# Optimization experiments

Hardware: AMD Instinct MI355X
Metric: run time of the kernel (lower is better)

Reference implementation:

```python
import jax, jax.numpy as jnp
import numpy as np

DIM = 128
HEADS = 4
K = 7          # neighborhood kernel size
MLP_RATIO = 4
EPS = 1e-5


def setup_inputs() -> dict:
    key = jax.random.key(0)
    ks = jax.random.split(key, 8)
    B, H, W, C = 4, 64, 64, DIM
    hid = C * MLP_RATIO
    s = lambda k, shape: jax.random.normal(k, shape, jnp.float32) * 0.02
    return {
        "x": jax.random.normal(ks[0], (B, H, W, C), jnp.float32),
        "ln1_g": jnp.ones((C,), jnp.float32),
        "ln1_b": jnp.zeros((C,), jnp.float32),
        "qkv_w": s(ks[1], (C, 3 * C)),
        "qkv_b": jnp.zeros((3 * C,), jnp.float32),
        "rpb": s(ks[2], (HEADS, 2 * K - 1, 2 * K - 1)),
        "proj_w": s(ks[3], (C, C)),
        "proj_b": jnp.zeros((C,), jnp.float32),
        "ln2_g": jnp.ones((C,), jnp.float32),
        "ln2_b": jnp.zeros((C,), jnp.float32),
        "fc1_w": s(ks[4], (C, hid)),
        "fc1_b": jnp.zeros((hid,), jnp.float32),
        "fc2_w": s(ks[5], (hid, C)),
        "fc2_b": jnp.zeros((C,), jnp.float32),
    }


def _ln(x, g, b):
    m = jnp.mean(x, axis=-1, keepdims=True)
    v = jnp.mean(jnp.square(x - m), axis=-1, keepdims=True)
    return (x - m) * jax.lax.rsqrt(v + EPS) * g + b


def _neigh_idx(L, k):
    # NATTEN border-clamped neighborhood: start = clamp(i - k//2, 0, L-k)
    i = jnp.arange(L)
    start = jnp.clip(i - k // 2, 0, L - k)
    idx = start[:, None] + jnp.arange(k)[None, :]        # [L, k] key positions
    rel = idx - i[:, None] + (k - 1)                     # [L, k] rpb indices in [0, 2k-2]
    return idx, rel


def _neighborhood_attention(x, qkv_w, qkv_b, rpb, proj_w, proj_b):
    B, H, W, C = x.shape
    nh, hd = HEADS, C // HEADS
    scale = hd ** -0.5
    qkv = (x @ qkv_w + qkv_b).reshape(B, H, W, 3, nh, hd)
    qkv = qkv.transpose(3, 0, 4, 1, 2, 5)                # [3, B, nh, H, W, hd]
    q, k_, v = qkv[0] * scale, qkv[1], qkv[2]
    ih, rh = _neigh_idx(H, K)
    iw, rw = _neigh_idx(W, K)
    # gather 7x7 neighborhoods: [B, nh, H, K, W, K, hd]
    kg = k_[:, :, ih][:, :, :, :, iw]
    vg = v[:, :, ih][:, :, :, :, iw]
    attn = jnp.einsum('bnywc,bnykxjc->bnyxkj', q, kg)    # [B, nh, H, W, K, K]
    bias = rpb[:, rh][:, :, :, rw]                       # [nh, H, K, W, K]
    attn = attn + bias.transpose(0, 1, 3, 2, 4)[None]
    a = jax.nn.softmax(attn.reshape(B, nh, H, W, K * K), axis=-1)
    a = a.reshape(B, nh, H, W, K, K)
    out = jnp.einsum('bnyxkj,bnykxjc->bnyxc', a, vg)     # [B, nh, H, W, hd]
    out = out.transpose(0, 2, 3, 1, 4).reshape(B, H, W, C)
    return out @ proj_w + proj_b


def reference(x, ln1_g, ln1_b, qkv_w, qkv_b, rpb, proj_w, proj_b,
              ln2_g, ln2_b, fc1_w, fc1_b, fc2_w, fc2_b):
    h = x + _neighborhood_attention(_ln(x, ln1_g, ln1_b), qkv_w, qkv_b, rpb, proj_w, proj_b)
    y = _ln(h, ln2_g, ln2_b)
    y = jax.nn.gelu(y @ fc1_w + fc1_b, approximate=False) @ fc2_w + fc2_b
    return h + y
```

## Files before the change

kernel.cpp:

```cpp
#include <hip/hip_runtime.h>
#include <math.h>

#define TOKS 16384
#define CDIM 128
#define NH 4
#define HD 32
#define HID 512
#define QSCALE 0.17677669529663687f
#define LEPS 1e-5f

typedef const float* fp;
typedef const unsigned short* bfp16;
typedef __attribute__((ext_vector_type(8))) short bf16x8;
typedef __attribute__((ext_vector_type(4))) float f32x4;

__device__ inline unsigned int bfp2(float a, float b) {
    unsigned int ua = __float_as_uint(a); ua = (ua + 0x7FFFu + ((ua >> 16) & 1u)) >> 16;
    unsigned int ub = __float_as_uint(b); ub = (ub + 0x7FFFu + ((ub >> 16) & 1u)) >> 16;
    return ua | (ub << 16);
}
__device__ inline unsigned short bf1(float a) {
    unsigned int u = __float_as_uint(a);
    return (unsigned short)((u + 0x7FFFu + ((u >> 16) & 1u)) >> 16);
}
__device__ inline float lo16(unsigned int u) { return __uint_as_float(u << 16); }
__device__ inline float hi16(unsigned int u) { return __uint_as_float(u & 0xFFFF0000u); }

__global__ __launch_bounds__(256) void prep(fp qw, fp pw, fp f1w, fp f2w,
                                            fp x, fp g, fp b,
                                            unsigned short* __restrict__ wt,
                                            unsigned short* __restrict__ xn) {
    const int bid = blockIdx.x;
    if (bid < 768) {
        int e = bid * 256 + threadIdx.x;
        float v;
        if (e < 49152)       { int n = e >> 7,  k = e & 127;          v = qw[(size_t)k * 384 + n]; }
        else if (e < 65536)  { int i = e - 49152;  int n = i >> 7, k = i & 127; v = pw[(size_t)k * 128 + n]; }
        else if (e < 131072) { int i = e - 65536;  int n = i >> 7, k = i & 127; v = f1w[(size_t)k * 512 + n]; }
        else                 { int i = e - 131072; int n = i >> 9, k = i & 511; v = f2w[(size_t)k * 128 + n]; }
        wt[e] = bf1(v);
    } else {
        const int t = threadIdx.x;
        const int row = (bid - 768) * 8 + (t >> 5);
        const int l = t & 31;
        const float4 v = *(const float4*)(x + (size_t)row * CDIM + l * 4);
        float s = v.x + v.y + v.z + v.w;
        float q = v.x * v.x + v.y * v.y + v.z * v.z + v.w * v.w;
#pragma unroll
        for (int m = 16; m >= 1; m >>= 1) { s += __shfl_xor(s, m); q += __shfl_xor(q, m); }
        float mu = s * (1.f / 128.f);
        float rs = rsqrtf(q * (1.f / 128.f) - mu * mu + LEPS);
        const float4 gv = *(const float4*)(g + l * 4);
        const float4 bv = *(const float4*)(b + l * 4);
        float a0 = (v.x - mu) * rs * gv.x + bv.x, a1 = (v.y - mu) * rs * gv.y + bv.y;
        float a2 = (v.z - mu) * rs * gv.z + bv.z, a3 = (v.w - mu) * rs * gv.w + bv.w;
        uint2 o; o.x = bfp2(a0, a1); o.y = bfp2(a2, a3);
        *(uint2*)(xn + (size_t)row * CDIM + l * 4) = o;
    }
}


__global__ __launch_bounds__(256) void k1_mfma(bfp16 xn, bfp16 wt0, fp wb,
                                               float* __restrict__ qb,
                                               unsigned short* __restrict__ kvb) {
    __shared__ unsigned int lds[12288];
    const int m0 = blockIdx.x * 128;
    const int nb = blockIdx.y * 64;
    const int tid = threadIdx.x;
#pragma unroll
    for (int i = 0; i < 8; i++) {
        int slot = tid + i * 256;
        int m = slot >> 4, c16 = slot & 15;
        const uint4 v4 = *(const uint4*)(xn + (size_t)(m0 + m) * CDIM + c16 * 8);
        *(uint4*)&lds[m * 64 + (c16 ^ (m & 15)) * 4] = v4;
    }
#pragma unroll
    for (int i = 0; i < 4; i++) {
        int slot = tid + i * 256;
        int n = slot >> 4, c16 = slot & 15;
        const uint4 v4 = *(const uint4*)(wt0 + (size_t)(nb + n) * 128 + c16 * 8);
        *(uint4*)&lds[8192 + n * 64 + (c16 ^ (n & 15)) * 4] = v4;
    }
    __syncthreads();

    const int lane = tid & 63, wid = tid >> 6, quad = lane >> 4, l16 = lane & 15;
    f32x4 acc[2][4];
#pragma unroll
    for (int mt = 0; mt < 2; mt++)
#pragma unroll
        for (int nt = 0; nt < 4; nt++) acc[mt][nt] = (f32x4){0.f, 0.f, 0.f, 0.f};
#pragma unroll
    for (int kk = 0; kk < 4; kk++) {
        int c = kk * 4 + quad;
        bf16x8 a0 = *(bf16x8*)&lds[(wid * 32 + l16) * 64 + (c ^ l16) * 4];
        bf16x8 a1 = *(bf16x8*)&lds[(wid * 32 + 16 + l16) * 64 + (c ^ l16) * 4];
#pragma unroll
        for (int nt = 0; nt < 4; nt++) {
            bf16x8 bf = *(bf16x8*)&lds[8192 + (nt * 16 + l16) * 64 + (c ^ l16) * 4];
            acc[0][nt] = __builtin_amdgcn_mfma_f32_16x16x32_bf16(a0, bf, acc[0][nt], 0, 0, 0);
            acc[1][nt] = __builtin_amdgcn_mfma_f32_16x16x32_bf16(a1, bf, acc[1][nt], 0, 0, 0);
        }
    }
#pragma unroll
    for (int nt = 0; nt < 4; nt++) {
        int col = nb + nt * 16 + l16;
        float bias = wb[col];
#pragma unroll
        for (int mt = 0; mt < 2; mt++)
#pragma unroll
            for (int r = 0; r < 4; r++) {
                int row = m0 + wid * 32 + mt * 16 + quad * 4 + r;
                float vres = acc[mt][nt][r] + bias;
                if (col < 128)
                    qb[(size_t)row * 128 + col] = vres * QSCALE;
                else if (col < 256)
                    kvb[(size_t)row * 256 + (col - 128)] = bf1(vres);
                else
                    kvb[(size_t)row * 256 + 128 + (col - 256)] = bf1(vres);
            }
    }
}

__global__ __launch_bounds__(256) void k2_attn(const float* __restrict__ qb,
                                               const unsigned short* __restrict__ kvb,
                                               fp rpb, unsigned short* __restrict__ attnb) {
    const int gid = blockIdx.x * 256 + threadIdx.x;
    const int d = gid & 3;
    const int g = (gid >> 2) & 3;
    const int head = (gid >> 4) & 3;
    const int token = gid >> 6;
    const int bb = token >> 12;
    const int y = (token >> 6) & 63;
    const int xx = token & 63;
    const int sy = min(max(y - 3, 0), 57);
    const int sx = min(max(xx - 3, 0), 57);

    const int koff = head * HD + d * 8;
    float q[8];
    {
        const float4* qp = (const float4*)(qb + (size_t)token * 128 + koff);
        float4 q0 = qp[0], q1 = qp[1];
        q[0] = q0.x; q[1] = q0.y; q[2] = q0.z; q[3] = q0.w;
        q[4] = q1.x; q[5] = q1.y; q[6] = q1.z; q[7] = q1.w;
    }

    const float* rp = rpb + head * 169 + (sy - y + 6) * 13 + (sx - xx + 6);
    const int nbase = (bb << 12) + sy * 64 + sx;

    float sc[13];
#pragma unroll
    for (int i = 0; i < 13; i++) {
        int n = g * 13 + i;
        bool ok = n < 49;
        int nn = ok ? n : 48;
        int dy = nn / 7, dx = nn - dy * 7;
        const uint4 kk = *(const uint4*)(kvb + (size_t)(nbase + dy * 64 + dx) * 256 + koff);
        float s = q[0] * lo16(kk.x) + q[1] * hi16(kk.x)
                + q[2] * lo16(kk.y) + q[3] * hi16(kk.y)
                + q[4] * lo16(kk.z) + q[5] * hi16(kk.z)
                + q[6] * lo16(kk.w) + q[7] * hi16(kk.w);
        s += __shfl_xor(s, 1);
        s += __shfl_xor(s, 2);
        sc[i] = ok ? (s + rp[dy * 13 + dx]) : -1e30f;
    }
    float mx = sc[0];
#pragma unroll
    for (int l = 1; l < 13; l++) mx = fmaxf(mx, sc[l]);
    mx = fmaxf(mx, __shfl_xor(mx, 4));
    mx = fmaxf(mx, __shfl_xor(mx, 8));
    float sum = 0.f;
#pragma unroll
    for (int l = 0; l < 13; l++) { sc[l] = __expf(sc[l] - mx); sum += sc[l]; }
    sum += __shfl_xor(sum, 4);
    sum += __shfl_xor(sum, 8);
    float inv = 1.f / sum;

    float o[8];
#pragma unroll
    for (int i = 0; i < 8; i++) o[i] = 0.f;
#pragma unroll
    for (int i = 0; i < 13; i++) {
        int n = g * 13 + i;
        int nn = (n < 49) ? n : 48;
        int dy = nn / 7, dx = nn - dy * 7;
        float p = sc[i] * inv;
        const uint4 vv = *(const uint4*)(kvb + (size_t)(nbase + dy * 64 + dx) * 256 + 128 + koff);
        o[0] += p * lo16(vv.x); o[1] += p * hi16(vv.x);
        o[2] += p * lo16(vv.y); o[3] += p * hi16(vv.y);
        o[4] += p * lo16(vv.z); o[5] += p * hi16(vv.z);
        o[6] += p * lo16(vv.w); o[7] += p * hi16(vv.w);
    }
#pragma unroll
    for (int i = 0; i < 8; i++) {
        o[i] += __shfl_xor(o[i], 4);
        o[i] += __shfl_xor(o[i], 8);
    }
    if (g == 0) {
        uint4 ov;
        ov.x = bfp2(o[0], o[1]); ov.y = bfp2(o[2], o[3]);
        ov.z = bfp2(o[4], o[5]); ov.w = bfp2(o[6], o[7]);
        *(uint4*)(attnb + (size_t)token * 128 + koff) = ov;
    }
}

__global__ __launch_bounds__(256) void k3_mfma(bfp16 attnb, fp x, bfp16 wt1, fp pb,
                                               fp g2, fp b2,
                                               float* __restrict__ h,
                                               unsigned short* __restrict__ hn) {
    __shared__ unsigned int lds[12288];
    const int m0 = blockIdx.x * 64;
    const int tid = threadIdx.x;
#pragma unroll
    for (int i = 0; i < 4; i++) {
        int slot = tid + i * 256;
        int m = slot >> 4, c16 = slot & 15;
        const uint4 v4 = *(const uint4*)(attnb + (size_t)(m0 + m) * CDIM + c16 * 8);
        *(uint4*)&lds[m * 64 + (c16 ^ (m & 15)) * 4] = v4;
    }
#pragma unroll
    for (int i = 0; i < 8; i++) {
        int slot = tid + i * 256;
        int n = slot >> 4, c16 = slot & 15;
        const uint4 v4 = *(const uint4*)(wt1 + (size_t)n * 128 + c16 * 8);
        *(uint4*)&lds[4096 + n * 64 + (c16 ^ (n & 15)) * 4] = v4;
    }
    __syncthreads();

    const int lane = tid & 63, wid = tid >> 6, quad = lane >> 4, l16 = lane & 15;
    const int mrow = wid * 16 + l16;
    f32x4 acc[8];
#pragma unroll
    for (int nt = 0; nt < 8; nt++) acc[nt] = (f32x4){0.f, 0.f, 0.f, 0.f};
#pragma unroll
    for (int kk = 0; kk < 4; kk++) {
        int c = kk * 4 + quad;
        bf16x8 a = *(bf16x8*)&lds[mrow * 64 + (c ^ l16) * 4];
#pragma unroll
        for (int nt = 0; nt < 8; nt++) {
            bf16x8 bf = *(bf16x8*)&lds[4096 + (nt * 16 + l16) * 64 + (c ^ l16) * 4];
            acc[nt] = __builtin_amdgcn_mfma_f32_16x16x32_bf16(a, bf, acc[nt], 0, 0, 0);
        }
    }
    float s[4] = {0.f, 0.f, 0.f, 0.f}, q[4] = {0.f, 0.f, 0.f, 0.f};
#pragma unroll
    for (int nt = 0; nt < 8; nt++) {
        int col = nt * 16 + l16;
        float bias = pb[col];
#pragma unroll
        for (int r = 0; r < 4; r++) {
            int row = m0 + wid * 16 + quad * 4 + r;
            float hv = x[(size_t)row * CDIM + col] + acc[nt][r] + bias;
            h[(size_t)row * CDIM + col] = hv;
            acc[nt][r] = hv;
            s[r] += hv; q[r] += hv * hv;
        }
    }
#pragma unroll
    for (int m = 1; m <= 8; m <<= 1) {
#pragma unroll
        for (int r = 0; r < 4; r++) {
            s[r] += __shfl_xor(s[r], m);
            q[r] += __shfl_xor(q[r], m);
        }
    }
    float mu[4], rs[4];
#pragma unroll
    for (int r = 0; r < 4; r++) {
        mu[r] = s[r] * (1.f / 128.f);
        rs[r] = rsqrtf(q[r] * (1.f / 128.f) - mu[r] * mu[r] + LEPS);
    }
#pragma unroll
    for (int nt = 0; nt < 8; nt++) {
        int col = nt * 16 + l16;
        float gg = g2[col], bb = b2[col];
#pragma unroll
        for (int r = 0; r < 4; r++) {
            int row = m0 + wid * 16 + quad * 4 + r;
            hn[(size_t)row * CDIM + col] = bf1((acc[nt][r] - mu[r]) * rs[r] * gg + bb);
        }
    }
}

__global__ __launch_bounds__(256) void k4_mfma(bfp16 hn, bfp16 wt2, fp wb,
                                               unsigned short* __restrict__ y1) {
    __shared__ unsigned int lds[12288];
    const int m0 = blockIdx.x * 128;
    const int nb = blockIdx.y * 64;
    const int tid = threadIdx.x;
#pragma unroll
    for (int i = 0; i < 8; i++) {
        int slot = tid + i * 256;
        int m = slot >> 4, c16 = slot & 15;
        const uint4 v4 = *(const uint4*)(hn + (size_t)(m0 + m) * CDIM + c16 * 8);
        *(uint4*)&lds[m * 64 + (c16 ^ (m & 15)) * 4] = v4;
    }
#pragma unroll
    for (int i = 0; i < 4; i++) {
        int slot = tid + i * 256;
        int n = slot >> 4, c16 = slot & 15;
        const uint4 v4 = *(const uint4*)(wt2 + (size_t)(nb + n) * 128 + c16 * 8);
        *(uint4*)&lds[8192 + n * 64 + (c16 ^ (n & 15)) * 4] = v4;
    }
    __syncthreads();

    const int lane = tid & 63, wid = tid >> 6, quad = lane >> 4, l16 = lane & 15;
    f32x4 acc[2][4];
#pragma unroll
    for (int mt = 0; mt < 2; mt++)
#pragma unroll
        for (int nt = 0; nt < 4; nt++) acc[mt][nt] = (f32x4){0.f, 0.f, 0.f, 0.f};
#pragma unroll
    for (int kk = 0; kk < 4; kk++) {
        int c = kk * 4 + quad;
        bf16x8 a0 = *(bf16x8*)&lds[(wid * 32 + l16) * 64 + (c ^ l16) * 4];
        bf16x8 a1 = *(bf16x8*)&lds[(wid * 32 + 16 + l16) * 64 + (c ^ l16) * 4];
#pragma unroll
        for (int nt = 0; nt < 4; nt++) {
            bf16x8 bf = *(bf16x8*)&lds[8192 + (nt * 16 + l16) * 64 + (c ^ l16) * 4];
            acc[0][nt] = __builtin_amdgcn_mfma_f32_16x16x32_bf16(a0, bf, acc[0][nt], 0, 0, 0);
            acc[1][nt] = __builtin_amdgcn_mfma_f32_16x16x32_bf16(a1, bf, acc[1][nt], 0, 0, 0);
        }
    }
#pragma unroll
    for (int nt = 0; nt < 4; nt++) {
        int col = nb + nt * 16 + l16;
        float bias = wb[col];
#pragma unroll
        for (int mt = 0; mt < 2; mt++)
#pragma unroll
            for (int r = 0; r < 4; r++) {
                int row = m0 + wid * 32 + mt * 16 + quad * 4 + r;
                float z = acc[mt][nt][r] + bias;
                y1[(size_t)row * HID + col] = bf1(0.5f * z * (1.f + erff(z * 0.70710678118654752f)));
            }
    }
}

__global__ __launch_bounds__(256) void k5_mfma(bfp16 y1, fp h, bfp16 wt3, fp wb,
                                               float* __restrict__ out) {
    __shared__ unsigned int lds[12288];
    const int m0 = blockIdx.x * 128;
    const int nb = blockIdx.y * 64;
    const int tid = threadIdx.x;
    const int lane = tid & 63, wid = tid >> 6, quad = lane >> 4, l16 = lane & 15;
    f32x4 acc[2][4];
#pragma unroll
    for (int mt = 0; mt < 2; mt++)
#pragma unroll
        for (int nt = 0; nt < 4; nt++) acc[mt][nt] = (f32x4){0.f, 0.f, 0.f, 0.f};

    for (int kc = 0; kc < 4; kc++) {
        if (kc) __syncthreads();
#pragma unroll
        for (int i = 0; i < 8; i++) {
            int slot = tid + i * 256;
            int m = slot >> 4, c16 = slot & 15;
            const uint4 v4 = *(const uint4*)(y1 + (size_t)(m0 + m) * HID + kc * 128 + c16 * 8);
            *(uint4*)&lds[m * 64 + (c16 ^ (m & 15)) * 4] = v4;
        }
#pragma unroll
        for (int i = 0; i < 4; i++) {
            int slot = tid + i * 256;
            int n = slot >> 4, c16 = slot & 15;
            const uint4 v4 = *(const uint4*)(wt3 + (size_t)(nb + n) * 512 + kc * 128 + c16 * 8);
            *(uint4*)&lds[8192 + n * 64 + (c16 ^ (n & 15)) * 4] = v4;
        }
        __syncthreads();
#pragma unroll
        for (int kk = 0; kk < 4; kk++) {
            int c = kk * 4 + quad;
            bf16x8 a0 = *(bf16x8*)&lds[(wid * 32 + l16) * 64 + (c ^ l16) * 4];
            bf16x8 a1 = *(bf16x8*)&lds[(wid * 32 + 16 + l16) * 64 + (c ^ l16) * 4];
#pragma unroll
            for (int nt = 0; nt < 4; nt++) {
                bf16x8 bf = *(bf16x8*)&lds[8192 + (nt * 16 + l16) * 64 + (c ^ l16) * 4];
                acc[0][nt] = __builtin_amdgcn_mfma_f32_16x16x32_bf16(a0, bf, acc[0][nt], 0, 0, 0);
                acc[1][nt] = __builtin_amdgcn_mfma_f32_16x16x32_bf16(a1, bf, acc[1][nt], 0, 0, 0);
            }
        }
    }
#pragma unroll
    for (int nt = 0; nt < 4; nt++) {
        int col = nb + nt * 16 + l16;
        float bias = wb[col];
#pragma unroll
        for (int mt = 0; mt < 2; mt++)
#pragma unroll
            for (int r = 0; r < 4; r++) {
                int row = m0 + wid * 32 + mt * 16 + quad * 4 + r;
                out[(size_t)row * CDIM + col] = h[(size_t)row * CDIM + col] + acc[mt][nt][r] + bias;
            }
    }
}

extern "C" void kernel_launch(void* const* d_in, const int* in_sizes, int n_in,
                              void* d_out, int out_size, void* d_ws, size_t ws_size,
                              hipStream_t stream) {
    fp x      = (fp)d_in[0];
    fp ln1_g  = (fp)d_in[1];
    fp ln1_b  = (fp)d_in[2];
    fp qkv_w  = (fp)d_in[3];
    fp qkv_b  = (fp)d_in[4];
    fp rpb    = (fp)d_in[5];
    fp proj_w = (fp)d_in[6];
    fp proj_b = (fp)d_in[7];
    fp ln2_g  = (fp)d_in[8];
    fp ln2_b  = (fp)d_in[9];
    fp fc1_w  = (fp)d_in[10];
    fp fc1_b  = (fp)d_in[11];
    fp fc2_w  = (fp)d_in[12];
    fp fc2_b  = (fp)d_in[13];
    float* out = (float*)d_out;

    float* ws = (float*)d_ws;
    float* h  = ws;
    unsigned short* xn = (unsigned short*)(h + (size_t)TOKS * CDIM);
    unsigned short* hn = xn + (size_t)TOKS * CDIM;
    float* qb = (float*)(hn + (size_t)TOKS * CDIM);
    unsigned short* kvb   = (unsigned short*)(qb + (size_t)TOKS * CDIM);
    unsigned short* attnb = kvb + (size_t)TOKS * 256;
    unsigned short* wt    = attnb + (size_t)TOKS * CDIM;
    unsigned short* y1    = (unsigned short*)qb;

    unsigned short* wt0 = wt;
    unsigned short* wt1 = wt + 49152;
    unsigned short* wt2 = wt + 65536;
    unsigned short* wt3 = wt + 131072;

    prep<<<768 + TOKS / 8, 256, 0, stream>>>(qkv_w, proj_w, fc1_w, fc2_w, x, ln1_g, ln1_b, wt, xn);
    k1_mfma<<<dim3(TOKS / 128, 6), 256, 0, stream>>>(xn, wt0, qkv_b, qb, kvb);
    k2_attn<<<TOKS * NH * 16 / 256, 256, 0, stream>>>(qb, kvb, rpb, attnb);
    k3_mfma<<<TOKS / 64, 256, 0, stream>>>(attnb, x, wt1, proj_b, ln2_g, ln2_b, h, hn);
    k4_mfma<<<dim3(TOKS / 128, 8), 256, 0, stream>>>(hn, wt2, fc1_b, y1);
    k5_mfma<<<dim3(TOKS / 128, 2), 256, 0, stream>>>(y1, h, wt3, fc2_b, out);
}
```

Before: 148.9 us.

## Fuse fc1+GELU and fc2 into one MLP kernel keeping hidden activations in LDS

Replaces the separate fc1+GELU and fc2 kernels with a single 512-thread kernel per 64-token tile. The GELU output for all 512 hidden channels stays in shared memory (swizzled), so the bf16 y1 intermediate is never written to or read from global memory. fc1 weight chunks are register-prefetched and double-buffered in LDS, and fc2 weight chunks are register-prefetched across the K loop. The cost is a large LDS footprint (112 KB per block) that limits occupancy, and every block now re-reads the full fc1 and fc2 weights.

Result: slower. 170.3 us (+14.4%).

```diff
diff --git a/kernel.cpp b/kernel.cpp
--- a/kernel.cpp
+++ b/kernel.cpp
@@ -59,7 +59,6 @@
     }
 }
 
-
 __global__ __launch_bounds__(256) void k1_mfma(bfp16 xn, bfp16 wt0, fp wb,
                                                float* __restrict__ qb,
                                                unsigned short* __restrict__ kvb) {
@@ -281,115 +280,124 @@
     }
 }
 
-__global__ __launch_bounds__(256) void k4_mfma(bfp16 hn, bfp16 wt2, fp wb,
-                                               unsigned short* __restrict__ y1) {
-    __shared__ unsigned int lds[12288];
-    const int m0 = blockIdx.x * 128;
-    const int nb = blockIdx.y * 64;
+__global__ __launch_bounds__(512) void kmlp(bfp16 hn, bfp16 wt2, fp b1, bfp16 wt3, fp b2,
+                                            fp h, float* __restrict__ out) {
+    __shared__ unsigned int lds[28672];
+    const int m0 = blockIdx.x * 64;
     const int tid = threadIdx.x;
 #pragma unroll
-    for (int i = 0; i < 8; i++) {
-        int slot = tid + i * 256;
+    for (int i = 0; i < 2; i++) {
+        int slot = tid + i * 512;
         int m = slot >> 4, c16 = slot & 15;
         const uint4 v4 = *(const uint4*)(hn + (size_t)(m0 + m) * CDIM + c16 * 8);
-        *(uint4*)&lds[m * 64 + (c16 ^ (m & 15)) * 4] = v4;
-    }
-#pragma unroll
-    for (int i = 0; i < 4; i++) {
-        int slot = tid + i * 256;
+        *(uint4*)&lds[m * 64 + ((c16 ^ (m & 15)) << 2)] = v4;
+    }
+#pragma unroll
+    for (int i = 0; i < 2; i++) {
+        int slot = tid + i * 512;
         int n = slot >> 4, c16 = slot & 15;
-        const uint4 v4 = *(const uint4*)(wt2 + (size_t)(nb + n) * 128 + c16 * 8);
-        *(uint4*)&lds[8192 + n * 64 + (c16 ^ (n & 15)) * 4] = v4;
+        const uint4 v4 = *(const uint4*)(wt2 + (size_t)n * 128 + c16 * 8);
+        *(uint4*)&lds[4096 + n * 64 + ((c16 ^ (n & 15)) << 2)] = v4;
     }
     __syncthreads();
 
     const int lane = tid & 63, wid = tid >> 6, quad = lane >> 4, l16 = lane & 15;
-    f32x4 acc[2][4];
-#pragma unroll
-    for (int mt = 0; mt < 2; mt++)
-#pragma unroll
-        for (int nt = 0; nt < 4; nt++) acc[mt][nt] = (f32x4){0.f, 0.f, 0.f, 0.f};
-#pragma unroll
-    for (int kk = 0; kk < 4; kk++) {
-        int c = kk * 4 + quad;
-        bf16x8 a0 = *(bf16x8*)&lds[(wid * 32 + l16) * 64 + (c ^ l16) * 4];
-        bf16x8 a1 = *(bf16x8*)&lds[(wid * 32 + 16 + l16) * 64 + (c ^ l16) * 4];
-#pragma unroll
-        for (int nt = 0; nt < 4; nt++) {
-            bf16x8 bf = *(bf16x8*)&lds[8192 + (nt * 16 + l16) * 64 + (c ^ l16) * 4];
-            acc[0][nt] = __builtin_amdgcn_mfma_f32_16x16x32_bf16(a0, bf, acc[0][nt], 0, 0, 0);
-            acc[1][nt] = __builtin_amdgcn_mfma_f32_16x16x32_bf16(a1, bf, acc[1][nt], 0, 0, 0);
-        }
-    }
-#pragma unroll
-    for (int nt = 0; nt < 4; nt++) {
-        int col = nb + nt * 16 + l16;
-        float bias = wb[col];
-#pragma unroll
-        for (int mt = 0; mt < 2; mt++)
-#pragma unroll
-            for (int r = 0; r < 4; r++) {
-                int row = m0 + wid * 32 + mt * 16 + quad * 4 + r;
-                float z = acc[mt][nt][r] + bias;
-                y1[(size_t)row * HID + col] = bf1(0.5f * z * (1.f + erff(z * 0.70710678118654752f)));
-            }
-    }
-}
-
-__global__ __launch_bounds__(256) void k5_mfma(bfp16 y1, fp h, bfp16 wt3, fp wb,
-                                               float* __restrict__ out) {
-    __shared__ unsigned int lds[12288];
-    const int m0 = blockIdx.x * 128;
-    const int nb = blockIdx.y * 64;
-    const int tid = threadIdx.x;
-    const int lane = tid & 63, wid = tid >> 6, quad = lane >> 4, l16 = lane & 15;
-    f32x4 acc[2][4];
-#pragma unroll
-    for (int mt = 0; mt < 2; mt++)
-#pragma unroll
-        for (int nt = 0; nt < 4; nt++) acc[mt][nt] = (f32x4){0.f, 0.f, 0.f, 0.f};
-
-    for (int kc = 0; kc < 4; kc++) {
-        if (kc) __syncthreads();
-#pragma unroll
-        for (int i = 0; i < 8; i++) {
-            int slot = tid + i * 256;
-            int m = slot >> 4, c16 = slot & 15;
-            const uint4 v4 = *(const uint4*)(y1 + (size_t)(m0 + m) * HID + kc * 128 + c16 * 8);
-            *(uint4*)&lds[m * 64 + (c16 ^ (m & 15)) * 4] = v4;
-        }
-#pragma unroll
-        for (int i = 0; i < 4; i++) {
-            int slot = tid + i * 256;
-            int n = slot >> 4, c16 = slot & 15;
-            const uint4 v4 = *(const uint4*)(wt3 + (size_t)(nb + n) * 512 + kc * 128 + c16 * 8);
-            *(uint4*)&lds[8192 + n * 64 + (c16 ^ (n & 15)) * 4] = v4;
-        }
-        __syncthreads();
+    const int ht = wid & 3;
+    const int tt0 = (wid >> 2) << 1;
+
+    for (int ch = 0; ch < 8; ch++) {
+        const int cur = 4096 + ((ch & 1) << 11);
+        uint4 pf0, pf1;
+        if (ch < 7) {
+            int s0 = tid, s1 = tid + 512;
+            pf0 = *(const uint4*)(wt2 + (size_t)((ch + 1) * 64 + (s0 >> 4)) * 128 + (s0 & 15) * 8);
+            pf1 = *(const uint4*)(wt2 + (size_t)((ch + 1) * 64 + (s1 >> 4)) * 128 + (s1 & 15) * 8);
+        }
+        f32x4 acc0 = (f32x4){0.f, 0.f, 0.f, 0.f}, acc1 = (f32x4){0.f, 0.f, 0.f, 0.f};
 #pragma unroll
         for (int kk = 0; kk < 4; kk++) {
             int c = kk * 4 + quad;
-            bf16x8 a0 = *(bf16x8*)&lds[(wid * 32 + l16) * 64 + (c ^ l16) * 4];
-            bf16x8 a1 = *(bf16x8*)&lds[(wid * 32 + 16 + l16) * 64 + (c ^ l16) * 4];
-#pragma unroll
-            for (int nt = 0; nt < 4; nt++) {
-                bf16x8 bf = *(bf16x8*)&lds[8192 + (nt * 16 + l16) * 64 + (c ^ l16) * 4];
-                acc[0][nt] = __builtin_amdgcn_mfma_f32_16x16x32_bf16(a0, bf, acc[0][nt], 0, 0, 0);
-                acc[1][nt] = __builtin_amdgcn_mfma_f32_16x16x32_bf16(a1, bf, acc[1][nt], 0, 0, 0);
+            bf16x8 wf = *(bf16x8*)&lds[cur + (ht * 16 + l16) * 64 + ((c ^ l16) << 2)];
+            bf16x8 x0 = *(bf16x8*)&lds[(tt0 * 16 + l16) * 64 + ((c ^ l16) << 2)];
+            bf16x8 x1 = *(bf16x8*)&lds[((tt0 + 1) * 16 + l16) * 64 + ((c ^ l16) << 2)];
+            acc0 = __builtin_amdgcn_mfma_f32_16x16x32_bf16(wf, x0, acc0, 0, 0, 0);
+            acc1 = __builtin_amdgcn_mfma_f32_16x16x32_bf16(wf, x1, acc1, 0, 0, 0);
+        }
+        const int hidb = ch * 64 + ht * 16 + quad * 4;
+        const float4 bb = *(const float4*)(b1 + hidb);
+        const int c16y = hidb >> 3;
+        const int woff = (quad & 1) << 1;
+#pragma unroll
+        for (int t = 0; t < 2; t++) {
+            f32x4 a = t ? acc1 : acc0;
+            int row = (tt0 + t) * 16 + l16;
+            float z0 = a[0] + bb.x, z1 = a[1] + bb.y, z2 = a[2] + bb.z, z3 = a[3] + bb.w;
+            float g0 = 0.5f * z0 * (1.f + erff(z0 * 0.70710678118654752f));
+            float g1 = 0.5f * z1 * (1.f + erff(z1 * 0.70710678118654752f));
+            float g2v = 0.5f * z2 * (1.f + erff(z2 * 0.70710678118654752f));
+            float g3 = 0.5f * z3 * (1.f + erff(z3 * 0.70710678118654752f));
+            uint2 val; val.x = bfp2(g0, g1); val.y = bfp2(g2v, g3);
+            *(uint2*)&lds[12288 + row * 256 + ((c16y ^ (row & 15)) << 2) + woff] = val;
+        }
+        if (ch < 7) {
+            int base = 4096 + (((ch + 1) & 1) << 11);
+            int s0 = tid, s1 = tid + 512;
+            *(uint4*)&lds[base + (s0 >> 4) * 64 + ((((s0 & 15) ^ ((s0 >> 4) & 15))) << 2)] = pf0;
+            *(uint4*)&lds[base + (s1 >> 4) * 64 + ((((s1 & 15) ^ ((s1 >> 4) & 15))) << 2)] = pf1;
+        }
+        __syncthreads();
+    }
+
+    const int mt = wid >> 1;
+    const int nb0 = (wid & 1) << 2;
+    f32x4 acc[4];
+#pragma unroll
+    for (int j = 0; j < 4; j++) acc[j] = (f32x4){0.f, 0.f, 0.f, 0.f};
+
+    uint4 wreg[4];
+#pragma unroll
+    for (int i = 0; i < 4; i++) {
+        int slot = tid + i * 512;
+        wreg[i] = *(const uint4*)(wt3 + (size_t)(slot >> 4) * 512 + (slot & 15) * 8);
+    }
+    for (int kc = 0; kc < 4; kc++) {
+#pragma unroll
+        for (int i = 0; i < 4; i++) {
+            int slot = tid + i * 512;
+            int n = slot >> 4, c16 = slot & 15;
+            *(uint4*)&lds[4096 + n * 64 + ((c16 ^ (n & 15)) << 2)] = wreg[i];
+        }
+        __syncthreads();
+        if (kc < 3) {
+#pragma unroll
+            for (int i = 0; i < 4; i++) {
+                int slot = tid + i * 512;
+                wreg[i] = *(const uint4*)(wt3 + (size_t)(slot >> 4) * 512 + (kc + 1) * 128 + (slot & 15) * 8);
             }
         }
-    }
-#pragma unroll
-    for (int nt = 0; nt < 4; nt++) {
-        int col = nb + nt * 16 + l16;
-        float bias = wb[col];
-#pragma unroll
-        for (int mt = 0; mt < 2; mt++)
-#pragma unroll
-            for (int r = 0; r < 4; r++) {
-                int row = m0 + wid * 32 + mt * 16 + quad * 4 + r;
-                out[(size_t)row * CDIM + col] = h[(size_t)row * CDIM + col] + acc[mt][nt][r] + bias;
+#pragma unroll
+        for (int kk = 0; kk < 4; kk++) {
+            int c = kk * 4 + quad;
+            int row = mt * 16 + l16;
+            int cc = kc * 16 + c;
+            bf16x8 a = *(bf16x8*)&lds[12288 + row * 256 + ((cc ^ l16) << 2)];
+#pragma unroll
+            for (int j = 0; j < 4; j++) {
+                bf16x8 bfr = *(bf16x8*)&lds[4096 + ((nb0 + j) * 16 + l16) * 64 + ((c ^ l16) << 2)];
+                acc[j] = __builtin_amdgcn_mfma_f32_16x16x32_bf16(a, bfr, acc[j], 0, 0, 0);
             }
+        }
+        __syncthreads();
+    }
+#pragma unroll
+    for (int j = 0; j < 4; j++) {
+        int col = (nb0 + j) * 16 + l16;
+        float bias = b2[col];
+#pragma unroll
+        for (int r = 0; r < 4; r++) {
+            int row = m0 + mt * 16 + quad * 4 + r;
+            out[(size_t)row * CDIM + col] = h[(size_t)row * CDIM + col] + acc[j][r] + bias;
+        }
     }
 }
 
@@ -420,7 +428,6 @@
     unsigned short* kvb   = (unsigned short*)(qb + (size_t)TOKS * CDIM);
     unsigned short* attnb = kvb + (size_t)TOKS * 256;
     unsigned short* wt    = attnb + (size_t)TOKS * CDIM;
-    unsigned short* y1    = (unsigned short*)qb;
 
     unsigned short* wt0 = wt;
     unsigned short* wt1 = wt + 49152;
@@ -431,6 +438,5 @@
     k1_mfma<<<dim3(TOKS / 128, 6), 256, 0, stream>>>(xn, wt0, qkv_b, qb, kvb);
     k2_attn<<<TOKS * NH * 16 / 256, 256, 0, stream>>>(qb, kvb, rpb, attnb);
     k3_mfma<<<TOKS / 64, 256, 0, stream>>>(attnb, x, wt1, proj_b, ln2_g, ln2_b, h, hn);
-    k4_mfma<<<dim3(TOKS / 128, 8), 256, 0, stream>>>(hn, wt2, fc1_b, y1);
-    k5_mfma<<<dim3(TOKS / 128, 2), 256, 0, stream>>>(y1, h, wt3, fc2_b, out);
-}
+    kmlp<<<TOKS / 64, 512, 0, stream>>>(hn, wt2, fc1_b, wt3, fc2_b, h, out);
+}
```

## Fuse LN1 into QKV GEMM and restructure MLP GEMMs to full-width row tiles

Applied to the files above, without the earlier changes.

LayerNorm1 moves out of the prep kernel and into k1, which normalizes its 64-row tile of x directly into LDS. k1 and k4 now use 512-thread blocks that keep the A tile resident and loop over all N chunks, double-buffering weight chunks through registers and LDS. k5 uses 64-row tiles covering all 128 output columns. The aim is to drop the xn round trip through global memory and the repeated A-tile reloads across grid columns, at the cost of fewer, longer blocks and more serialized per-block work.

Result: slower. 153.5 us (+3.1%).

```diff
diff --git a/kernel.cpp b/kernel.cpp
--- a/kernel.cpp
+++ b/kernel.cpp
@@ -27,90 +27,91 @@
 __device__ inline float hi16(unsigned int u) { return __uint_as_float(u & 0xFFFF0000u); }
 
 __global__ __launch_bounds__(256) void prep(fp qw, fp pw, fp f1w, fp f2w,
-                                            fp x, fp g, fp b,
-                                            unsigned short* __restrict__ wt,
-                                            unsigned short* __restrict__ xn) {
-    const int bid = blockIdx.x;
-    if (bid < 768) {
-        int e = bid * 256 + threadIdx.x;
-        float v;
-        if (e < 49152)       { int n = e >> 7,  k = e & 127;          v = qw[(size_t)k * 384 + n]; }
-        else if (e < 65536)  { int i = e - 49152;  int n = i >> 7, k = i & 127; v = pw[(size_t)k * 128 + n]; }
-        else if (e < 131072) { int i = e - 65536;  int n = i >> 7, k = i & 127; v = f1w[(size_t)k * 512 + n]; }
-        else                 { int i = e - 131072; int n = i >> 9, k = i & 511; v = f2w[(size_t)k * 128 + n]; }
-        wt[e] = bf1(v);
-    } else {
-        const int t = threadIdx.x;
-        const int row = (bid - 768) * 8 + (t >> 5);
-        const int l = t & 31;
-        const float4 v = *(const float4*)(x + (size_t)row * CDIM + l * 4);
-        float s = v.x + v.y + v.z + v.w;
-        float q = v.x * v.x + v.y * v.y + v.z * v.z + v.w * v.w;
-#pragma unroll
-        for (int m = 16; m >= 1; m >>= 1) { s += __shfl_xor(s, m); q += __shfl_xor(q, m); }
-        float mu = s * (1.f / 128.f);
-        float rs = rsqrtf(q * (1.f / 128.f) - mu * mu + LEPS);
-        const float4 gv = *(const float4*)(g + l * 4);
-        const float4 bv = *(const float4*)(b + l * 4);
-        float a0 = (v.x - mu) * rs * gv.x + bv.x, a1 = (v.y - mu) * rs * gv.y + bv.y;
-        float a2 = (v.z - mu) * rs * gv.z + bv.z, a3 = (v.w - mu) * rs * gv.w + bv.w;
-        uint2 o; o.x = bfp2(a0, a1); o.y = bfp2(a2, a3);
-        *(uint2*)(xn + (size_t)row * CDIM + l * 4) = o;
-    }
-}
-
-
-__global__ __launch_bounds__(256) void k1_mfma(bfp16 xn, bfp16 wt0, fp wb,
+                                            unsigned short* __restrict__ wt) {
+    int e = blockIdx.x * 256 + threadIdx.x;
+    float v;
+    if (e < 49152)       { int n = e >> 7,  k = e & 127;          v = qw[(size_t)k * 384 + n]; }
+    else if (e < 65536)  { int i = e - 49152;  int n = i >> 7, k = i & 127; v = pw[(size_t)k * 128 + n]; }
+    else if (e < 131072) { int i = e - 65536;  int n = i >> 7, k = i & 127; v = f1w[(size_t)k * 512 + n]; }
+    else                 { int i = e - 131072; int n = i >> 9, k = i & 511; v = f2w[(size_t)k * 128 + n]; }
+    wt[e] = bf1(v);
+}
+
+__global__ __launch_bounds__(512) void k1_mfma(fp x, fp g1, fp b1, bfp16 wt0, fp wb,
                                                float* __restrict__ qb,
                                                unsigned short* __restrict__ kvb) {
     __shared__ unsigned int lds[12288];
-    const int m0 = blockIdx.x * 128;
-    const int nb = blockIdx.y * 64;
+    const int m0 = blockIdx.x * 64;
     const int tid = threadIdx.x;
 #pragma unroll
-    for (int i = 0; i < 8; i++) {
-        int slot = tid + i * 256;
+    for (int i = 0; i < 2; i++) {
+        int slot = tid + i * 512;
         int m = slot >> 4, c16 = slot & 15;
-        const uint4 v4 = *(const uint4*)(xn + (size_t)(m0 + m) * CDIM + c16 * 8);
-        *(uint4*)&lds[m * 64 + (c16 ^ (m & 15)) * 4] = v4;
-    }
-#pragma unroll
-    for (int i = 0; i < 4; i++) {
-        int slot = tid + i * 256;
-        int n = slot >> 4, c16 = slot & 15;
-        const uint4 v4 = *(const uint4*)(wt0 + (size_t)(nb + n) * 128 + c16 * 8);
-        *(uint4*)&lds[8192 + n * 64 + (c16 ^ (n & 15)) * 4] = v4;
-    }
-    __syncthreads();
-
+        const float4 v0 = *(const float4*)(x + (size_t)(m0 + m) * CDIM + c16 * 8);
+        const float4 v1 = *(const float4*)(x + (size_t)(m0 + m) * CDIM + c16 * 8 + 4);
+        float s = v0.x + v0.y + v0.z + v0.w + v1.x + v1.y + v1.z + v1.w;
+        float q = v0.x * v0.x + v0.y * v0.y + v0.z * v0.z + v0.w * v0.w
+                + v1.x * v1.x + v1.y * v1.y + v1.z * v1.z + v1.w * v1.w;
+#pragma unroll
+        for (int mm = 8; mm >= 1; mm >>= 1) { s += __shfl_xor(s, mm); q += __shfl_xor(q, mm); }
+        float mu = s * (1.f / 128.f);
+        float rs = rsqrtf(q * (1.f / 128.f) - mu * mu + LEPS);
+        const float4 ga = *(const float4*)(g1 + c16 * 8);
+        const float4 gb = *(const float4*)(g1 + c16 * 8 + 4);
+        const float4 ba = *(const float4*)(b1 + c16 * 8);
+        const float4 bb = *(const float4*)(b1 + c16 * 8 + 4);
+        uint4 o;
+        o.x = bfp2((v0.x - mu) * rs * ga.x + ba.x, (v0.y - mu) * rs * ga.y + ba.y);
+        o.y = bfp2((v0.z - mu) * rs * ga.z + ba.z, (v0.w - mu) * rs * ga.w + ba.w);
+        o.z = bfp2((v1.x - mu) * rs * gb.x + bb.x, (v1.y - mu) * rs * gb.y + bb.y);
+        o.w = bfp2((v1.z - mu) * rs * gb.z + bb.z, (v1.w - mu) * rs * gb.w + bb.w);
+        *(uint4*)&lds[m * 64 + ((c16 ^ (m & 15)) << 2)] = o;
+    }
+    uint4 wreg[2];
+#pragma unroll
+    for (int i = 0; i < 2; i++) {
+        int slot = tid + i * 512;
+        wreg[i] = *(const uint4*)(wt0 + (size_t)(slot >> 4) * 128 + (slot & 15) * 8);
+    }
     const int lane = tid & 63, wid = tid >> 6, quad = lane >> 4, l16 = lane & 15;
-    f32x4 acc[2][4];
-#pragma unroll
-    for (int mt = 0; mt < 2; mt++)
-#pragma unroll
-        for (int nt = 0; nt < 4; nt++) acc[mt][nt] = (f32x4){0.f, 0.f, 0.f, 0.f};
-#pragma unroll
-    for (int kk = 0; kk < 4; kk++) {
-        int c = kk * 4 + quad;
-        bf16x8 a0 = *(bf16x8*)&lds[(wid * 32 + l16) * 64 + (c ^ l16) * 4];
-        bf16x8 a1 = *(bf16x8*)&lds[(wid * 32 + 16 + l16) * 64 + (c ^ l16) * 4];
-#pragma unroll
-        for (int nt = 0; nt < 4; nt++) {
-            bf16x8 bf = *(bf16x8*)&lds[8192 + (nt * 16 + l16) * 64 + (c ^ l16) * 4];
-            acc[0][nt] = __builtin_amdgcn_mfma_f32_16x16x32_bf16(a0, bf, acc[0][nt], 0, 0, 0);
-            acc[1][nt] = __builtin_amdgcn_mfma_f32_16x16x32_bf16(a1, bf, acc[1][nt], 0, 0, 0);
-        }
-    }
-#pragma unroll
-    for (int nt = 0; nt < 4; nt++) {
-        int col = nb + nt * 16 + l16;
-        float bias = wb[col];
-#pragma unroll
-        for (int mt = 0; mt < 2; mt++)
+    const int mf = wid >> 1, nh = wid & 1;
+    for (int nc = 0; nc < 6; nc++) {
+        const int bse = 4096 + ((nc & 1) << 12);
+#pragma unroll
+        for (int i = 0; i < 2; i++) {
+            int slot = tid + i * 512;
+            int n = slot >> 4, c16 = slot & 15;
+            *(uint4*)&lds[bse + n * 64 + ((c16 ^ (n & 15)) << 2)] = wreg[i];
+        }
+        __syncthreads();
+        if (nc < 5) {
+#pragma unroll
+            for (int i = 0; i < 2; i++) {
+                int slot = tid + i * 512;
+                wreg[i] = *(const uint4*)(wt0 + (size_t)((nc + 1) * 64 + (slot >> 4)) * 128 + (slot & 15) * 8);
+            }
+        }
+        f32x4 acc[2];
+        acc[0] = (f32x4){0.f, 0.f, 0.f, 0.f};
+        acc[1] = (f32x4){0.f, 0.f, 0.f, 0.f};
+#pragma unroll
+        for (int kk = 0; kk < 4; kk++) {
+            int c = kk * 4 + quad;
+            bf16x8 a = *(bf16x8*)&lds[(mf * 16 + l16) * 64 + ((c ^ l16) << 2)];
+#pragma unroll
+            for (int nt = 0; nt < 2; nt++) {
+                bf16x8 bf = *(bf16x8*)&lds[bse + (nh * 32 + nt * 16 + l16) * 64 + ((c ^ l16) << 2)];
+                acc[nt] = __builtin_amdgcn_mfma_f32_16x16x32_bf16(a, bf, acc[nt], 0, 0, 0);
+            }
+        }
+#pragma unroll
+        for (int nt = 0; nt < 2; nt++) {
+            int col = nc * 64 + nh * 32 + nt * 16 + l16;
+            float bias = wb[col];
 #pragma unroll
             for (int r = 0; r < 4; r++) {
-                int row = m0 + wid * 32 + mt * 16 + quad * 4 + r;
-                float vres = acc[mt][nt][r] + bias;
+                int row = m0 + mf * 16 + quad * 4 + r;
+                float vres = acc[nt][r] + bias;
                 if (col < 128)
                     qb[(size_t)row * 128 + col] = vres * QSCALE;
                 else if (col < 256)
@@ -118,6 +119,7 @@
                 else
                     kvb[(size_t)row * 256 + 128 + (col - 256)] = bf1(vres);
             }
+        }
     }
 }
 
@@ -281,115 +283,116 @@
     }
 }
 
-__global__ __launch_bounds__(256) void k4_mfma(bfp16 hn, bfp16 wt2, fp wb,
+__global__ __launch_bounds__(512) void k4_mfma(bfp16 hn, bfp16 wt2, fp wb,
                                                unsigned short* __restrict__ y1) {
     __shared__ unsigned int lds[12288];
-    const int m0 = blockIdx.x * 128;
-    const int nb = blockIdx.y * 64;
+    const int m0 = blockIdx.x * 64;
     const int tid = threadIdx.x;
 #pragma unroll
-    for (int i = 0; i < 8; i++) {
-        int slot = tid + i * 256;
+    for (int i = 0; i < 2; i++) {
+        int slot = tid + i * 512;
         int m = slot >> 4, c16 = slot & 15;
         const uint4 v4 = *(const uint4*)(hn + (size_t)(m0 + m) * CDIM + c16 * 8);
-        *(uint4*)&lds[m * 64 + (c16 ^ (m & 15)) * 4] = v4;
-    }
-#pragma unroll
-    for (int i = 0; i < 4; i++) {
-        int slot = tid + i * 256;
-        int n = slot >> 4, c16 = slot & 15;
-        const uint4 v4 = *(const uint4*)(wt2 + (size_t)(nb + n) * 128 + c16 * 8);
-        *(uint4*)&lds[8192 + n * 64 + (c16 ^ (n & 15)) * 4] = v4;
-    }
-    __syncthreads();
-
+        *(uint4*)&lds[m * 64 + ((c16 ^ (m & 15)) << 2)] = v4;
+    }
+    uint4 wreg[2];
+#pragma unroll
+    for (int i = 0; i < 2; i++) {
+        int slot = tid + i * 512;
+        wreg[i] = *(const uint4*)(wt2 + (size_t)(slot >> 4) * 128 + (slot & 15) * 8);
+    }
     const int lane = tid & 63, wid = tid >> 6, quad = lane >> 4, l16 = lane & 15;
-    f32x4 acc[2][4];
-#pragma unroll
-    for (int mt = 0; mt < 2; mt++)
-#pragma unroll
-        for (int nt = 0; nt < 4; nt++) acc[mt][nt] = (f32x4){0.f, 0.f, 0.f, 0.f};
-#pragma unroll
-    for (int kk = 0; kk < 4; kk++) {
-        int c = kk * 4 + quad;
-        bf16x8 a0 = *(bf16x8*)&lds[(wid * 32 + l16) * 64 + (c ^ l16) * 4];
-        bf16x8 a1 = *(bf16x8*)&lds[(wid * 32 + 16 + l16) * 64 + (c ^ l16) * 4];
-#pragma unroll
-        for (int nt = 0; nt < 4; nt++) {
-            bf16x8 bf = *(bf16x8*)&lds[8192 + (nt * 16 + l16) * 64 + (c ^ l16) * 4];
-            acc[0][nt] = __builtin_amdgcn_mfma_f32_16x16x32_bf16(a0, bf, acc[0][nt], 0, 0, 0);
-            acc[1][nt] = __builtin_amdgcn_mfma_f32_16x16x32_bf16(a1, bf, acc[1][nt], 0, 0, 0);
-        }
-    }
-#pragma unroll
-    for (int nt = 0; nt < 4; nt++) {
-        int col = nb + nt * 16 + l16;
-        float bias = wb[col];
-#pragma unroll
-        for (int mt = 0; mt < 2; mt++)
+    const int mf = wid >> 1, nh = wid & 1;
+    for (int nc = 0; nc < 8; nc++) {
+        const int bse = 4096 + ((nc & 1) << 12);
+#pragma unroll
+        for (int i = 0; i < 2; i++) {
+            int slot = tid + i * 512;
+            int n = slot >> 4, c16 = slot & 15;
+            *(uint4*)&lds[bse + n * 64 + ((c16 ^ (n & 15)) << 2)] = wreg[i];
+        }
+        __syncthreads();
+        if (nc < 7) {
+#pragma unroll
+            for (int i = 0; i < 2; i++) {
+                int slot = tid + i * 512;
+                wreg[i] = *(const uint4*)(wt2 + (size_t)((nc + 1) * 64 + (slot >> 4)) * 128 + (slot & 15) * 8);
+            }
+        }
+        f32x4 acc[2];
+        acc[0] = (f32x4){0.f, 0.f, 0.f, 0.f};
+        acc[1] = (f32x4){0.f, 0.f, 0.f, 0.f};
+#pragma unroll
+        for (int kk = 0; kk < 4; kk++) {
+            int c = kk * 4 + quad;
+            bf16x8 a = *(bf16x8*)&lds[(mf * 16 + l16) * 64 + ((c ^ l16) << 2)];
+#pragma unroll
+            for (int nt = 0; nt < 2; nt++) {
+                bf16x8 bf = *(bf16x8*)&lds[bse + (nh * 32 + nt * 16 + l16) * 64 + ((c ^ l16) << 2)];
+                acc[nt] = __builtin_amdgcn_mfma_f32_16x16x32_bf16(a, bf, acc[nt], 0, 0, 0);
+            }
+        }
+#pragma unroll
+        for (int nt = 0; nt < 2; nt++) {
+            int col = nc * 64 + nh * 32 + nt * 16 + l16;
+            float bias = wb[col];
 #pragma unroll
             for (int r = 0; r < 4; r++) {
-                int row = m0 + wid * 32 + mt * 16 + quad * 4 + r;
-                float z = acc[mt][nt][r] + bias;
+                int row = m0 + mf * 16 + quad * 4 + r;
+                float z = acc[nt][r] + bias;
                 y1[(size_t)row * HID + col] = bf1(0.5f * z * (1.f + erff(z * 0.70710678118654752f)));
             }
+        }
     }
 }
 
 __global__ __launch_bounds__(256) void k5_mfma(bfp16 y1, fp h, bfp16 wt3, fp wb,
                                                float* __restrict__ out) {
     __shared__ unsigned int lds[12288];
-    const int m0 = blockIdx.x * 128;
-    const int nb = blockIdx.y * 64;
+    const int m0 = blockIdx.x * 64;
     const int tid = threadIdx.x;
     const int lane = tid & 63, wid = tid >> 6, quad = lane >> 4, l16 = lane & 15;
-    f32x4 acc[2][4];
-#pragma unroll
-    for (int mt = 0; mt < 2; mt++)
-#pragma unroll
-        for (int nt = 0; nt < 4; nt++) acc[mt][nt] = (f32x4){0.f, 0.f, 0.f, 0.f};
+    f32x4 acc[8];
+#pragma unroll
+    for (int nt = 0; nt < 8; nt++) acc[nt] = (f32x4){0.f, 0.f, 0.f, 0.f};
 
     for (int kc = 0; kc < 4; kc++) {
         if (kc) __syncthreads();
 #pragma unroll
-        for (int i = 0; i < 8; i++) {
+        for (int i = 0; i < 4; i++) {
             int slot = tid + i * 256;
             int m = slot >> 4, c16 = slot & 15;
             const uint4 v4 = *(const uint4*)(y1 + (size_t)(m0 + m) * HID + kc * 128 + c16 * 8);
-            *(uint4*)&lds[m * 64 + (c16 ^ (m & 15)) * 4] = v4;
-        }
-#pragma unroll
-        for (int i = 0; i < 4; i++) {
+            *(uint4*)&lds[m * 64 + ((c16 ^ (m & 15)) << 2)] = v4;
+        }
+#pragma unroll
+        for (int i = 0; i < 8; i++) {
             int slot = tid + i * 256;
             int n = slot >> 4, c16 = slot & 15;
-            const uint4 v4 = *(const uint4*)(wt3 + (size_t)(nb + n) * 512 + kc * 128 + c16 * 8);
-            *(uint4*)&lds[8192 + n * 64 + (c16 ^ (n & 15)) * 4] = v4;
+            const uint4 v4 = *(const uint4*)(wt3 + (size_t)n * 512 + kc * 128 + c16 * 8);
+            *(uint4*)&lds[4096 + n * 64 + ((c16 ^ (n & 15)) << 2)] = v4;
         }
         __syncthreads();
 #pragma unroll
         for (int kk = 0; kk < 4; kk++) {
             int c = kk * 4 + quad;
-            bf16x8 a0 = *(bf16x8*)&lds[(wid * 32 + l16) * 64 + (c ^ l16) * 4];
-            bf16x8 a1 = *(bf16x8*)&lds[(wid * 32 + 16 + l16) * 64 + (c ^ l16) * 4];
-#pragma unroll
-            for (int nt = 0; nt < 4; nt++) {
-                bf16x8 bf = *(bf16x8*)&lds[8192 + (nt * 16 + l16) * 64 + (c ^ l16) * 4];
-                acc[0][nt] = __builtin_amdgcn_mfma_f32_16x16x32_bf16(a0, bf, acc[0][nt], 0, 0, 0);
-                acc[1][nt] = __builtin_amdgcn_mfma_f32_16x16x32_bf16(a1, bf, acc[1][nt], 0, 0, 0);
-            }
-        }
-    }
-#pragma unroll
-    for (int nt = 0; nt < 4; nt++) {
-        int col = nb + nt * 16 + l16;
+            bf16x8 a = *(bf16x8*)&lds[(wid * 16 + l16) * 64 + ((c ^ l16) << 2)];
+#pragma unroll
+            for (int nt = 0; nt < 8; nt++) {
+                bf16x8 bf = *(bf16x8*)&lds[4096 + (nt * 16 + l16) * 64 + ((c ^ l16) << 2)];
+                acc[nt] = __builtin_amdgcn_mfma_f32_16x16x32_bf16(a, bf, acc[nt], 0, 0, 0);
+            }
+        }
+    }
+#pragma unroll
+    for (int nt = 0; nt < 8; nt++) {
+        int col = nt * 16 + l16;
         float bias = wb[col];
 #pragma unroll
-        for (int mt = 0; mt < 2; mt++)
-#pragma unroll
-            for (int r = 0; r < 4; r++) {
-                int row = m0 + wid * 32 + mt * 16 + quad * 4 + r;
-                out[(size_t)row * CDIM + col] = h[(size_t)row * CDIM + col] + acc[mt][nt][r] + bias;
-            }
+        for (int r = 0; r < 4; r++) {
+            int row = m0 + wid * 16 + quad * 4 + r;
+            out[(size_t)row * CDIM + col] = h[(size_t)row * CDIM + col] + acc[nt][r] + bias;
+        }
     }
 }
 
@@ -427,10 +430,10 @@
     unsigned short* wt2 = wt + 65536;
     unsigned short* wt3 = wt + 131072;
 
-    prep<<<768 + TOKS / 8, 256, 0, stream>>>(qkv_w, proj_w, fc1_w, fc2_w, x, ln1_g, ln1_b, wt, xn);
-    k1_mfma<<<dim3(TOKS / 128, 6), 256, 0, stream>>>(xn, wt0, qkv_b, qb, kvb);
+    prep<<<768, 256, 0, stream>>>(qkv_w, proj_w, fc1_w, fc2_w, wt);
+    k1_mfma<<<TOKS / 64, 512, 0, stream>>>(x, ln1_g, ln1_b, wt0, qkv_b, qb, kvb);
     k2_attn<<<TOKS * NH * 16 / 256, 256, 0, stream>>>(qb, kvb, rpb, attnb);
     k3_mfma<<<TOKS / 64, 256, 0, stream>>>(attnb, x, wt1, proj_b, ln2_g, ln2_b, h, hn);
-    k4_mfma<<<dim3(TOKS / 128, 8), 256, 0, stream>>>(hn, wt2, fc1_b, y1);
-    k5_mfma<<<dim3(TOKS / 128, 2), 256, 0, stream>>>(y1, h, wt3, fc2_b, out);
-}
+    k4_mfma<<<TOKS / 64, 512, 0, stream>>>(hn, wt2, fc1_b, y1);
+    k5_mfma<<<TOKS / 64, 256, 0, stream>>>(y1, h, wt3, fc2_b, out);
+}
```

## Tile neighborhood attention over 8x8 query blocks with K/V halo staged in LDS

Applied to the files above, without the earlier changes.

Rewrites the attention kernel so each 512-thread block handles an 8x8 tile of queries. It first stages the 14x14 K/V halo into swizzled shared memory, then each thread pair computes one head with an online softmax over the 7 rows of the window. This replaces many redundant global K/V gathers with shared-memory reads and cuts cross-lane reductions. In exchange it uses about 100KB of LDS per block, which limits occupancy, and each block must wait on a synchronised load phase.

Result: no change. 146.7 us (-1.5%).

```diff
diff --git a/kernel.cpp b/kernel.cpp
--- a/kernel.cpp
+++ b/kernel.cpp
@@ -59,7 +59,6 @@
     }
 }
 
-
 __global__ __launch_bounds__(256) void k1_mfma(bfp16 xn, bfp16 wt0, fp wb,
                                                float* __restrict__ qb,
                                                unsigned short* __restrict__ kvb) {
@@ -121,86 +120,112 @@
     }
 }
 
-__global__ __launch_bounds__(256) void k2_attn(const float* __restrict__ qb,
+__global__ __launch_bounds__(512) void k2_attn(const float* __restrict__ qb,
                                                const unsigned short* __restrict__ kvb,
                                                fp rpb, unsigned short* __restrict__ attnb) {
-    const int gid = blockIdx.x * 256 + threadIdx.x;
-    const int d = gid & 3;
-    const int g = (gid >> 2) & 3;
-    const int head = (gid >> 4) & 3;
-    const int token = gid >> 6;
-    const int bb = token >> 12;
-    const int y = (token >> 6) & 63;
-    const int xx = token & 63;
+    __shared__ unsigned int lds[25088];
+    const int tile = blockIdx.x;
+    const int bb = tile >> 6;
+    const int ty0 = ((tile >> 3) & 7) << 3;
+    const int tx0 = (tile & 7) << 3;
+    const int ry0 = min(max(ty0 - 3, 0), 50);
+    const int rx0 = min(max(tx0 - 3, 0), 50);
+    const int tid = threadIdx.x;
+
+#pragma unroll
+    for (int it = 0; it < 13; it++) {
+        int slot = it * 512 + tid;
+        if (slot < 6272) {
+            int r = slot >> 5, c = slot & 31;
+            int i = r / 14, j = r - i * 14;
+            const uint4 v = *(const uint4*)(kvb + (size_t)((bb << 12) + (ry0 + i) * 64 + rx0 + j) * 256 + c * 8);
+            *(uint4*)&lds[r * 128 + ((c ^ (r & 7)) << 2)] = v;
+        }
+    }
+
+    const int dh = tid & 1;
+    const int head = (tid >> 1) & 3;
+    const int t = tid >> 3;
+    const int tx = t & 7, ty = t >> 3;
+    const int y = ty0 + ty, x = tx0 + tx;
+    const int token = (bb << 12) + y * 64 + x;
     const int sy = min(max(y - 3, 0), 57);
-    const int sx = min(max(xx - 3, 0), 57);
-
-    const int koff = head * HD + d * 8;
-    float q[8];
+    const int sx = min(max(x - 3, 0), 57);
+    const int ib = sy - ry0, jb = sx - rx0;
+    const float* rp = rpb + head * 169 + (sy - y + 6) * 13 + (sx - x + 6);
+
+    float q[16];
     {
-        const float4* qp = (const float4*)(qb + (size_t)token * 128 + koff);
-        float4 q0 = qp[0], q1 = qp[1];
-        q[0] = q0.x; q[1] = q0.y; q[2] = q0.z; q[3] = q0.w;
-        q[4] = q1.x; q[5] = q1.y; q[6] = q1.z; q[7] = q1.w;
-    }
-
-    const float* rp = rpb + head * 169 + (sy - y + 6) * 13 + (sx - xx + 6);
-    const int nbase = (bb << 12) + sy * 64 + sx;
-
-    float sc[13];
-#pragma unroll
-    for (int i = 0; i < 13; i++) {
-        int n = g * 13 + i;
-        bool ok = n < 49;
-        int nn = ok ? n : 48;
-        int dy = nn / 7, dx = nn - dy * 7;
-        const uint4 kk = *(const uint4*)(kvb + (size_t)(nbase + dy * 64 + dx) * 256 + koff);
-        float s = q[0] * lo16(kk.x) + q[1] * hi16(kk.x)
-                + q[2] * lo16(kk.y) + q[3] * hi16(kk.y)
-                + q[4] * lo16(kk.z) + q[5] * hi16(kk.z)
-                + q[6] * lo16(kk.w) + q[7] * hi16(kk.w);
-        s += __shfl_xor(s, 1);
-        s += __shfl_xor(s, 2);
-        sc[i] = ok ? (s + rp[dy * 13 + dx]) : -1e30f;
-    }
-    float mx = sc[0];
-#pragma unroll
-    for (int l = 1; l < 13; l++) mx = fmaxf(mx, sc[l]);
-    mx = fmaxf(mx, __shfl_xor(mx, 4));
-    mx = fmaxf(mx, __shfl_xor(mx, 8));
-    float sum = 0.f;
-#pragma unroll
-    for (int l = 0; l < 13; l++) { sc[l] = __expf(sc[l] - mx); sum += sc[l]; }
-    sum += __shfl_xor(sum, 4);
-    sum += __shfl_xor(sum, 8);
-    float inv = 1.f / sum;
-
-    float o[8];
-#pragma unroll
-    for (int i = 0; i < 8; i++) o[i] = 0.f;
-#pragma unroll
-    for (int i = 0; i < 13; i++) {
-        int n = g * 13 + i;
-        int nn = (n < 49) ? n : 48;
-        int dy = nn / 7, dx = nn - dy * 7;
-        float p = sc[i] * inv;
-        const uint4 vv = *(const uint4*)(kvb + (size_t)(nbase + dy * 64 + dx) * 256 + 128 + koff);
-        o[0] += p * lo16(vv.x); o[1] += p * hi16(vv.x);
-        o[2] += p * lo16(vv.y); o[3] += p * hi16(vv.y);
-        o[4] += p * lo16(vv.z); o[5] += p * hi16(vv.z);
-        o[6] += p * lo16(vv.w); o[7] += p * hi16(vv.w);
-    }
-#pragma unroll
-    for (int i = 0; i < 8; i++) {
-        o[i] += __shfl_xor(o[i], 4);
-        o[i] += __shfl_xor(o[i], 8);
-    }
-    if (g == 0) {
-        uint4 ov;
-        ov.x = bfp2(o[0], o[1]); ov.y = bfp2(o[2], o[3]);
-        ov.z = bfp2(o[4], o[5]); ov.w = bfp2(o[6], o[7]);
-        *(uint4*)(attnb + (size_t)token * 128 + koff) = ov;
-    }
+        const float4* qp = (const float4*)(qb + (size_t)token * 128 + head * 32 + dh * 16);
+        float4 a = qp[0], b = qp[1], c = qp[2], d = qp[3];
+        q[0] = a.x; q[1] = a.y; q[2] = a.z; q[3] = a.w;
+        q[4] = b.x; q[5] = b.y; q[6] = b.z; q[7] = b.w;
+        q[8] = c.x; q[9] = c.y; q[10] = c.z; q[11] = c.w;
+        q[12] = d.x; q[13] = d.y; q[14] = d.z; q[15] = d.w;
+    }
+    __syncthreads();
+
+    const int cb = (head << 2) + (dh << 1);
+    float m = -1e30f, l = 0.f;
+    float o[16];
+#pragma unroll
+    for (int i2 = 0; i2 < 16; i2++) o[i2] = 0.f;
+
+    for (int dy = 0; dy < 7; dy++) {
+        float s[7];
+#pragma unroll
+        for (int dx = 0; dx < 7; dx++) {
+            int r = (ib + dy) * 14 + jb + dx;
+            int sw = r & 7;
+            const uint4 k0 = *(const uint4*)&lds[r * 128 + ((cb ^ sw) << 2)];
+            const uint4 k1 = *(const uint4*)&lds[r * 128 + (((cb + 1) ^ sw) << 2)];
+            float ss = q[0] * lo16(k0.x) + q[1] * hi16(k0.x)
+                     + q[2] * lo16(k0.y) + q[3] * hi16(k0.y)
+                     + q[4] * lo16(k0.z) + q[5] * hi16(k0.z)
+                     + q[6] * lo16(k0.w) + q[7] * hi16(k0.w)
+                     + q[8] * lo16(k1.x) + q[9] * hi16(k1.x)
+                     + q[10] * lo16(k1.y) + q[11] * hi16(k1.y)
+                     + q[12] * lo16(k1.z) + q[13] * hi16(k1.z)
+                     + q[14] * lo16(k1.w) + q[15] * hi16(k1.w);
+            ss += __shfl_xor(ss, 1);
+            s[dx] = ss + rp[dy * 13 + dx];
+        }
+        float rm = s[0];
+#pragma unroll
+        for (int dx = 1; dx < 7; dx++) rm = fmaxf(rm, s[dx]);
+        float mn = fmaxf(m, rm);
+        float cf = __expf(m - mn);
+        l *= cf;
+#pragma unroll
+        for (int i2 = 0; i2 < 16; i2++) o[i2] *= cf;
+#pragma unroll
+        for (int dx = 0; dx < 7; dx++) {
+            int r = (ib + dy) * 14 + jb + dx;
+            int sw = r & 7;
+            const uint4 v0 = *(const uint4*)&lds[r * 128 + (((cb + 16) ^ sw) << 2)];
+            const uint4 v1 = *(const uint4*)&lds[r * 128 + (((cb + 17) ^ sw) << 2)];
+            float p = __expf(s[dx] - mn);
+            l += p;
+            o[0] += p * lo16(v0.x); o[1] += p * hi16(v0.x);
+            o[2] += p * lo16(v0.y); o[3] += p * hi16(v0.y);
+            o[4] += p * lo16(v0.z); o[5] += p * hi16(v0.z);
+            o[6] += p * lo16(v0.w); o[7] += p * hi16(v0.w);
+            o[8] += p * lo16(v1.x); o[9] += p * hi16(v1.x);
+            o[10] += p * lo16(v1.y); o[11] += p * hi16(v1.y);
+            o[12] += p * lo16(v1.z); o[13] += p * hi16(v1.z);
+            o[14] += p * lo16(v1.w); o[15] += p * hi16(v1.w);
+        }
+        m = mn;
+    }
+    float inv = 1.f / l;
+    unsigned short* op = attnb + (size_t)token * 128 + head * 32 + dh * 16;
+    uint4 ov;
+    ov.x = bfp2(o[0] * inv, o[1] * inv); ov.y = bfp2(o[2] * inv, o[3] * inv);
+    ov.z = bfp2(o[4] * inv, o[5] * inv); ov.w = bfp2(o[6] * inv, o[7] * inv);
+    *(uint4*)op = ov;
+    ov.x = bfp2(o[8] * inv, o[9] * inv); ov.y = bfp2(o[10] * inv, o[11] * inv);
+    ov.z = bfp2(o[12] * inv, o[13] * inv); ov.w = bfp2(o[14] * inv, o[15] * inv);
+    *(uint4*)(op + 8) = ov;
 }
 
 __global__ __launch_bounds__(256) void k3_mfma(bfp16 attnb, fp x, bfp16 wt1, fp pb,
@@ -429,7 +454,7 @@
 
     prep<<<768 + TOKS / 8, 256, 0, stream>>>(qkv_w, proj_w, fc1_w, fc2_w, x, ln1_g, ln1_b, wt, xn);
     k1_mfma<<<dim3(TOKS / 128, 6), 256, 0, stream>>>(xn, wt0, qkv_b, qb, kvb);
-    k2_attn<<<TOKS * NH * 16 / 256, 256, 0, stream>>>(qb, kvb, rpb, attnb);
+    k2_attn<<<TOKS / 64, 512, 0, stream>>>(qb, kvb, rpb, attnb);
     k3_mfma<<<TOKS / 64, 256, 0, stream>>>(attnb, x, wt1, proj_b, ln2_g, ln2_b, h, hn);
     k4_mfma<<<dim3(TOKS / 128, 8), 256, 0, stream>>>(hn, wt2, fc1_b, y1);
     k5_mfma<<<dim3(TOKS / 128, 2), 256, 0, stream>>>(y1, h, wt3, fc2_b, out);
```
